# Kernel optimization log

Hardware: AMD Instinct MI355X
Metric: run time of the kernel (lower is better)

Reference implementation:

```python
import jax, jax.numpy as jnp
import numpy as np

DIM = 2048
N_HEADS = 32
N_KV_HEADS = 8
HEAD_DIM = DIM // N_HEADS  # 64
MAX_SEQ_LEN = 2048
ROPE_THETA = 10000.0
ROPE_SCALE = 1.0  # ("linear", 1.0)


def build_rope_cache(seq_len):
    # standard half-rotation RoPE cache with linear position scaling
    inv_freq = 1.0 / (ROPE_THETA ** (jnp.arange(0, HEAD_DIM, 2, dtype=jnp.float32) / HEAD_DIM))
    t = jnp.arange(seq_len, dtype=jnp.float32) / ROPE_SCALE
    freqs = jnp.outer(t, inv_freq)                      # [S, HD/2]
    emb = jnp.concatenate([freqs, freqs], axis=-1)      # [S, HD]
    return jnp.cos(emb), jnp.sin(emb)


def apply_rope(x, cos, sin):
    # x: [B, S, H, D]; cos/sin: [S, D]
    c = cos[None, :, None, :]
    s = sin[None, :, None, :]
    x1, x2 = jnp.split(x, 2, axis=-1)
    rot = jnp.concatenate([-x2, x1], axis=-1)           # rotate_half
    return x * c + rot * s


def setup_inputs() -> dict:
    key = jax.random.key(0)
    kx, kq, kk, kv, ko = jax.random.split(key, 5)
    B, S = 1, 2048
    x = jax.random.normal(kx, (B, S, DIM), dtype=jnp.float32)
    # nn.Linear weights stored [out_features, in_features]
    wq = jax.random.normal(kq, (DIM, DIM), dtype=jnp.float32) * 0.02
    wk = jax.random.normal(kk, (HEAD_DIM * N_KV_HEADS, DIM), dtype=jnp.float32) * 0.02
    wv = jax.random.normal(kv, (HEAD_DIM * N_KV_HEADS, DIM), dtype=jnp.float32) * 0.02
    wo = jax.random.normal(ko, (DIM, DIM), dtype=jnp.float32) * 0.02
    return {"x": x, "wq": wq, "wk": wk, "wv": wv, "wo": wo}


def reference(x, wq, wk, wv, wo):
    B, S, _ = x.shape
    g = N_HEADS // N_KV_HEADS  # GQA expand factor
    q = (x @ wq.T).reshape(B, S, N_HEADS, HEAD_DIM)
    k = (x @ wk.T).reshape(B, S, N_KV_HEADS, HEAD_DIM)
    v = (x @ wv.T).reshape(B, S, N_KV_HEADS, HEAD_DIM)
    cos, sin = build_rope_cache(S)
    q = apply_rope(q, cos, sin)
    k = apply_rope(k, cos, sin)
    # group q heads with their kv head instead of repeat_interleave on k/v
    q = q.transpose(0, 2, 1, 3).reshape(B, N_KV_HEADS, g, S, HEAD_DIM)
    k = k.transpose(0, 2, 1, 3)   # [B, Hkv, S, D]
    v = v.transpose(0, 2, 1, 3)
    scale = 1.0 / jnp.sqrt(jnp.asarray(HEAD_DIM, dtype=x.dtype))
    scores = jnp.einsum('bhgqd,bhkd->bhgqk', q, k) * scale  # [B,Hkv,g,S,S]
    causal = jnp.tril(jnp.ones((S, S), dtype=bool))
    scores = jnp.where(causal[None, None, None, :, :], scores, -jnp.inf)
    p = jax.nn.softmax(scores, axis=-1)
    out = jnp.einsum('bhgqk,bhkd->bhgqd', p, v)             # [B,Hkv,g,S,D]
    out = out.reshape(B, N_HEADS, S, HEAD_DIM).transpose(0, 2, 1, 3).reshape(B, S, DIM)
    return out @ wo.T
```

## Files before the change

### kernel.cpp

```cpp
#include <hip/hip_runtime.h>
#include <hip/hip_bf16.h>
#include <cstdint>
#include <cstddef>

#define DIM_ 2048
#define SLEN 2048
#define NQH 32
#define NKVH 8
#define HDIM 64
#define KVDIM 512

typedef __attribute__((ext_vector_type(8))) short short8;
typedef __attribute__((ext_vector_type(4))) float f32x4;
typedef __attribute__((ext_vector_type(16))) float f32x16;
typedef __attribute__((ext_vector_type(4))) unsigned int u32x4;

#define QSCALE 0.1803368801111243f

__device__ __forceinline__ unsigned short f2bf(float f) {
  unsigned u = __builtin_bit_cast(unsigned, f);
  u += 0x7FFFu + ((u >> 16) & 1u);
  return (unsigned short)(u >> 16);
}

__device__ __forceinline__ unsigned cvt_pk_bf16(float lo, float hi) {
  unsigned r;
  asm("v_cvt_pk_bf16_f32 %0, %1, %2" : "=v"(r) : "v"(lo), "v"(hi));
  return r;
}

__device__ __forceinline__ void gload_lds16(const void* g, void* l) {
  __builtin_amdgcn_global_load_lds(
      (const __attribute__((address_space(1))) void*)g,
      (__attribute__((address_space(3))) void*)l, 16, 0, 0);
}

__global__ void cvt_bf16_kernel(const float* __restrict__ in,
                                unsigned short* __restrict__ out, int n) {
  int i = (blockIdx.x * blockDim.x + threadIdx.x) * 8;
  if (i >= n) return;
  float4 a = *(const float4*)(in + i);
  float4 b = *(const float4*)(in + i + 4);
  ushort4 o0, o1;
  o0.x = f2bf(a.x); o0.y = f2bf(a.y); o0.z = f2bf(a.z); o0.w = f2bf(a.w);
  o1.x = f2bf(b.x); o1.y = f2bf(b.y); o1.z = f2bf(b.z); o1.w = f2bf(b.w);
  *(ushort4*)(out + i) = o0;
  *(ushort4*)(out + i + 4) = o1;
}

__global__ void rope_table_kernel(float* __restrict__ cosT, float* __restrict__ sinT) {
  int idx = blockIdx.x * blockDim.x + threadIdx.x;
  int s = idx >> 5, i = idx & 31;
  float inv = expf(-(float)i * (9.210340371976184f / 32.0f));
  float fr = (float)s * inv;
  cosT[idx] = cosf(fr);
  sinT[idx] = sinf(fr);
}

__global__ __launch_bounds__(512, 2)
void gemm_qkv(const unsigned short* __restrict__ A,
              const unsigned short* __restrict__ B,
              unsigned short* __restrict__ Qr,
              unsigned short* __restrict__ Kr,
              unsigned short* __restrict__ Vtp,
              const float* __restrict__ cosT,
              const float* __restrict__ sinT) {
  constexpr int K = DIM_;
  __shared__ unsigned short sA[128 * 32];
  __shared__ unsigned short sB[128 * 32];
  const int tid = threadIdx.x;
  const int wv = tid >> 6, ln = tid & 63;
  const int row0 = blockIdx.x * 128;
  const int col0 = blockIdx.y * 128;
  const int wr = (wv >> 1) * 32, wc = (wv & 1) * 64;
  const int lrow = ln & 15, lk = (ln >> 4) * 8;
  const int rr = tid >> 2, cc = (tid & 3) * 8;
  f32x4 acc[2][4] = {};

  for (int kt = 0; kt < K; kt += 32) {
    gload_lds16(A + (size_t)(row0 + rr) * K + kt + cc, sA + wv * 512);
    gload_lds16(B + (size_t)(col0 + rr) * K + kt + cc, sB + wv * 512);
    __syncthreads();
    short8 af[2], bfr[4];
#pragma unroll
    for (int m = 0; m < 2; ++m)
      af[m] = *(const short8*)(sA + (wr + m * 16 + lrow) * 32 + lk);
#pragma unroll
    for (int n = 0; n < 4; ++n)
      bfr[n] = *(const short8*)(sB + (wc + n * 16 + lrow) * 32 + lk);
#pragma unroll
    for (int m = 0; m < 2; ++m)
#pragma unroll
      for (int n = 0; n < 4; ++n)
        acc[m][n] = __builtin_amdgcn_mfma_f32_16x16x32_bf16(af[m], bfr[n],
                                                            acc[m][n], 0, 0, 0);
    __syncthreads();
  }
  const int orow = (ln >> 4) * 4;
  const int by = blockIdx.y;
  if (by < 16) {
#pragma unroll
    for (int m = 0; m < 2; ++m)
#pragma unroll
      for (int j = 0; j < 4; ++j) {
        const int s = row0 + wr + m * 16 + orow + j;
#pragma unroll
        for (int n = 0; n < 2; ++n) {
          const int d1 = n * 16 + lrow;
          const float cv = cosT[s * 32 + d1], sv = sinT[s * 32 + d1];
          const float x1 = acc[m][n][j], x2 = acc[m][n + 2][j];
          const size_t base = (size_t)s * DIM_ + col0 + wc + d1;
          Qr[base] = f2bf((x1 * cv - x2 * sv) * QSCALE);
          Qr[base + 32] = f2bf((x2 * cv + x1 * sv) * QSCALE);
        }
      }
  } else if (by < 20) {
    const int cb = col0 - 2048;
#pragma unroll
    for (int m = 0; m < 2; ++m)
#pragma unroll
      for (int j = 0; j < 4; ++j) {
        const int s = row0 + wr + m * 16 + orow + j;
#pragma unroll
        for (int n = 0; n < 2; ++n) {
          const int d1 = n * 16 + lrow;
          const float cv = cosT[s * 32 + d1], sv = sinT[s * 32 + d1];
          const float x1 = acc[m][n][j], x2 = acc[m][n + 2][j];
          const size_t base = (size_t)s * KVDIM + cb + wc + d1;
          Kr[base] = f2bf(x1 * cv - x2 * sv);
          Kr[base + 32] = f2bf(x2 * cv + x1 * sv);
        }
      }
  } else {
    const int cb = col0 - 2560;
#pragma unroll
    for (int m = 0; m < 2; ++m)
#pragma unroll
      for (int n = 0; n < 4; ++n)
#pragma unroll
        for (int j = 0; j < 4; ++j) {
          const int s = row0 + wr + m * 16 + orow + j;
          const int vc = cb + wc + n * 16 + lrow;
          Vtp[(size_t)vc * SLEN + s] = f2bf(acc[m][n][j]);
        }
  }
}

__global__ __launch_bounds__(512, 2)
void gemm_bt_f32(const unsigned short* __restrict__ A,
                 const unsigned short* __restrict__ B, float* __restrict__ C) {
  constexpr int K = DIM_;
  __shared__ unsigned short sA[128 * 32];
  __shared__ unsigned short sB[128 * 32];
  const int tid = threadIdx.x;
  const int wv = tid >> 6, ln = tid & 63;
  const int row0 = blockIdx.x * 128;
  const int col0 = blockIdx.y * 128;
  const int wr = (wv >> 1) * 32, wc = (wv & 1) * 64;
  const int lrow = ln & 15, lk = (ln >> 4) * 8;
  const int rr = tid >> 2, cc = (tid & 3) * 8;
  f32x4 acc[2][4] = {};
  for (int kt = 0; kt < K; kt += 32) {
    gload_lds16(A + (size_t)(row0 + rr) * K + kt + cc, sA + wv * 512);
    gload_lds16(B + (size_t)(col0 + rr) * K + kt + cc, sB + wv * 512);
    __syncthreads();
    short8 af[2], bfr[4];
#pragma unroll
    for (int m = 0; m < 2; ++m)
      af[m] = *(const short8*)(sA + (wr + m * 16 + lrow) * 32 + lk);
#pragma unroll
    for (int n = 0; n < 4; ++n)
      bfr[n] = *(const short8*)(sB + (wc + n * 16 + lrow) * 32 + lk);
#pragma unroll
    for (int m = 0; m < 2; ++m)
#pragma unroll
      for (int n = 0; n < 4; ++n)
        acc[m][n] = __builtin_amdgcn_mfma_f32_16x16x32_bf16(af[m], bfr[n],
                                                            acc[m][n], 0, 0, 0);
    __syncthreads();
  }
  const int orow = (ln >> 4) * 4;
#pragma unroll
  for (int m = 0; m < 2; ++m)
#pragma unroll
    for (int n = 0; n < 4; ++n)
#pragma unroll
      for (int j = 0; j < 4; ++j)
        C[(size_t)(row0 + wr + m * 16 + orow + j) * DIM_ + col0 + wc + n * 16 + lrow] =
            acc[m][n][j];
}

__global__ __launch_bounds__(256, 3)
void attn3_kernel(const unsigned short* __restrict__ Q,
                  const unsigned short* __restrict__ Kc,
                  const unsigned short* __restrict__ Vt,
                  unsigned short* __restrict__ AO) {
  __shared__ __align__(16) char smem[32768];
  const int c = 15 - blockIdx.x, h = blockIdx.y;
  const int kvh = h >> 2;
  const int tid = threadIdx.x;
  const int w = tid >> 6, l = tid & 63;
  const int l31 = l & 31, hi = l >> 5;
  const int kvcol = kvh * HDIM;
  const int nt = (c + 1) * 2;
  const int wq0 = c * 128 + w * 32;
  const int qrow = wq0 + l31;

  int srow[2], scolb[2];
#pragma unroll
  for (int r = 0; r < 2; ++r) {
    int L = (r * 256 + tid) * 16;
    int row = L >> 7;
    srow[r] = row;
    scolb[r] = (L & 127) ^ ((row & 7) << 4);
  }

  short8 qf[4];
  {
    const unsigned short* qp = Q + (size_t)qrow * DIM_ + h * HDIM + hi * 8;
#pragma unroll
    for (int dblk = 0; dblk < 4; ++dblk) qf[dblk] = *(const short8*)(qp + dblk * 16);
  }
  f32x16 o[2] = {};
  float mrun = -1e30f, lrun = 0.f;

#pragma unroll
  for (int r = 0; r < 2; ++r) {
    gload_lds16((const char*)Kc + (((size_t)srow[r] * KVDIM + kvcol) << 1) + scolb[r],
                smem + r * 4096 + w * 1024);
    gload_lds16((const char*)Vt + (((size_t)(kvcol + srow[r]) * SLEN) << 1) + scolb[r],
                smem + 16384 + r * 4096 + w * 1024);
  }
  __syncthreads();

  for (int t = 0; t < nt; ++t) {
    const int cur = t & 1;
    const int k0 = t * 64;
    if (t + 1 < nt) {
      const int nb = cur ^ 1;
      const int k0n = k0 + 64;
#pragma unroll
      for (int r = 0; r < 2; ++r) {
        gload_lds16((const char*)Kc + (((size_t)(k0n + srow[r]) * KVDIM + kvcol) << 1) + scolb[r],
                    smem + nb * 8192 + r * 4096 + w * 1024);
        gload_lds16((const char*)Vt + (((size_t)(kvcol + srow[r]) * SLEN + k0n) << 1) + scolb[r],
                    smem + 16384 + nb * 8192 + r * 4096 + w * 1024);
      }
    }
    if (k0 <= wq0 + 31) {
      const char* sK = smem + cur * 8192;
      const char* sV = smem + 16384 + cur * 8192;
      f32x16 s0 = {}, s1 = {};
      __builtin_amdgcn_s_setprio(1);
#pragma unroll
      for (int dblk = 0; dblk < 4; ++dblk) {
        const int colb = (dblk * 32 + hi * 16) ^ ((l31 & 7) << 4);
        short8 kf0 = *(const short8*)(sK + l31 * 128 + colb);
        short8 kf1 = *(const short8*)(sK + (32 + l31) * 128 + colb);
        s0 = __builtin_amdgcn_mfma_f32_32x32x16_bf16(kf0, qf[dblk], s0, 0, 0, 0);
        s1 = __builtin_amdgcn_mfma_f32_32x32x16_bf16(kf1, qf[dblk], s1, 0, 0, 0);
      }
      __builtin_amdgcn_s_setprio(0);

      float p[32];
#pragma unroll
      for (int r = 0; r < 16; ++r) { p[r] = s0[r]; p[16 + r] = s1[r]; }
      if (k0 + 63 > wq0) {
#pragma unroll
        for (int r = 0; r < 16; ++r) {
          const int ka = k0 + (r & 3) + 8 * (r >> 2) + 4 * hi;
          if (ka > qrow) p[r] = -1e30f;
          if (ka + 32 > qrow) p[16 + r] = -1e30f;
        }
      }
      float t16[16];
#pragma unroll
      for (int i = 0; i < 16; ++i) t16[i] = fmaxf(p[i], p[i + 16]);
#pragma unroll
      for (int i = 0; i < 8; ++i) t16[i] = fmaxf(t16[i], t16[i + 8]);
#pragma unroll
      for (int i = 0; i < 4; ++i) t16[i] = fmaxf(t16[i], t16[i + 4]);
      float pmax = fmaxf(fmaxf(t16[0], t16[1]), fmaxf(t16[2], t16[3]));
      pmax = fmaxf(pmax, __shfl_xor(pmax, 32));
      if (!__all(pmax - mrun <= 8.0f)) {
        const float mnew = fmaxf(mrun, pmax);
        const float alpha = exp2f(mrun - mnew);
        mrun = mnew;
        lrun *= alpha;
#pragma unroll
        for (int r = 0; r < 16; ++r) { o[0][r] *= alpha; o[1][r] *= alpha; }
      }
#pragma unroll
      for (int i = 0; i < 32; ++i) p[i] = exp2f(p[i] - mrun);
      float u16[16];
#pragma unroll
      for (int i = 0; i < 16; ++i) u16[i] = p[i] + p[i + 16];
#pragma unroll
      for (int i = 0; i < 8; ++i) u16[i] += u16[i + 8];
#pragma unroll
      for (int i = 0; i < 4; ++i) u16[i] += u16[i + 4];
      float rs = (u16[0] + u16[1]) + (u16[2] + u16[3]);
      rs += __shfl_xor(rs, 32);
      lrun += rs;

      unsigned pa[8], pb[8];
#pragma unroll
      for (int i = 0; i < 8; ++i) {
        pa[i] = cvt_pk_bf16(p[i * 4 + 0], p[i * 4 + 1]);
        pb[i] = cvt_pk_bf16(p[i * 4 + 2], p[i * 4 + 3]);
      }
      __builtin_amdgcn_s_setprio(1);
#pragma unroll
      for (int kb = 0; kb < 4; ++kb) {
        const int i0 = (kb >> 1) * 4 + (kb & 1) * 2;
        const int i1 = i0 + 1;
        unsigned w0 = pa[i0], w2 = pa[i1];
        asm("v_permlane32_swap_b32 %0, %1" : "+v"(w0), "+v"(w2));
        unsigned w1 = pb[i0], w3 = pb[i1];
        asm("v_permlane32_swap_b32 %0, %1" : "+v"(w1), "+v"(w3));
        u32x4 uu = {w0, w1, w2, w3};
        short8 pf = __builtin_bit_cast(short8, uu);
        const int colb = (kb * 32 + hi * 16) ^ ((l31 & 7) << 4);
        short8 vf0 = *(const short8*)(sV + l31 * 128 + colb);
        short8 vf1 = *(const short8*)(sV + (32 + l31) * 128 + colb);
        o[0] = __builtin_amdgcn_mfma_f32_32x32x16_bf16(vf0, pf, o[0], 0, 0, 0);
        o[1] = __builtin_amdgcn_mfma_f32_32x32x16_bf16(vf1, pf, o[1], 0, 0, 0);
      }
      __builtin_amdgcn_s_setprio(0);
    }
    __syncthreads();
  }

  const float inv = 1.0f / lrun;
  char* tw = smem + w * 4096;
#pragma unroll
  for (int db = 0; db < 2; ++db)
#pragma unroll
    for (int g = 0; g < 4; ++g) {
      ushort4 v;
      v.x = f2bf(o[db][g * 4 + 0] * inv);
      v.y = f2bf(o[db][g * 4 + 1] * inv);
      v.z = f2bf(o[db][g * 4 + 2] * inv);
      v.w = f2bf(o[db][g * 4 + 3] * inv);
      const int d0 = db * 32 + g * 8 + hi * 4;
      *(ushort4*)(tw + l31 * 128 + ((d0 * 2) ^ ((l31 & 7) << 4))) = v;
    }
  {
    const int rr = l >> 1, cc = (l & 1) * 32;
    unsigned short* ap = AO + (size_t)(c * 128 + w * 32 + rr) * DIM_ + h * HDIM + cc;
#pragma unroll
    for (int pq = 0; pq < 4; ++pq) {
      const int colb = ((cc + pq * 8) * 2) ^ ((rr & 7) << 4);
      short8 v = *(const short8*)(tw + rr * 128 + colb);
      *(short8*)(ap + pq * 8) = v;
    }
  }
}

extern "C" void kernel_launch(void* const* d_in, const int* in_sizes, int n_in,
                              void* d_out, int out_size, void* d_ws, size_t ws_size,
                              hipStream_t stream) {
  const float* x  = (const float*)d_in[0];
  const float* wq = (const float*)d_in[1];
  const float* wk = (const float*)d_in[2];
  const float* wv = (const float*)d_in[3];
  const float* wo = (const float*)d_in[4];
  float* out = (float*)d_out;
  char* ws = (char*)d_ws;
  const size_t MB = 1u << 20;
  unsigned short* bx   = (unsigned short*)(ws + 0 * MB);
  unsigned short* bqkv = (unsigned short*)(ws + 8 * MB);
  unsigned short* bwo  = (unsigned short*)(ws + 20 * MB);
  unsigned short* Qr   = (unsigned short*)(ws + 28 * MB);
  unsigned short* Kr   = (unsigned short*)(ws + 36 * MB);
  unsigned short* Vt   = (unsigned short*)(ws + 38 * MB);
  unsigned short* AO   = (unsigned short*)(ws + 40 * MB);
  float* cosT = (float*)(ws + 48 * MB);
  float* sinT = (float*)(ws + 48 * MB + 256 * 1024);

  rope_table_kernel<<<SLEN * 32 / 256, 256, 0, stream>>>(cosT, sinT);
  cvt_bf16_kernel<<<(2048 * 2048 / 8) / 256, 256, 0, stream>>>(x, bx, 2048 * 2048);
  cvt_bf16_kernel<<<(2048 * 2048 / 8) / 256, 256, 0, stream>>>(wq, bqkv, 2048 * 2048);
  cvt_bf16_kernel<<<(512 * 2048 / 8) / 256, 256, 0, stream>>>(wk, bqkv + 2048 * 2048, 512 * 2048);
  cvt_bf16_kernel<<<(512 * 2048 / 8) / 256, 256, 0, stream>>>(wv, bqkv + 2560 * 2048, 512 * 2048);
  cvt_bf16_kernel<<<(2048 * 2048 / 8) / 256, 256, 0, stream>>>(wo, bwo, 2048 * 2048);

  gemm_qkv<<<dim3(16, 24), 512, 0, stream>>>(bx, bqkv, Qr, Kr, Vt, cosT, sinT);

  attn3_kernel<<<dim3(16, 32), 256, 0, stream>>>(Qr, Kr, Vt, AO);

  gemm_bt_f32<<<dim3(16, 16), 512, 0, stream>>>(AO, bwo, out);
}
```

Measured before the change: 257.5 us.

## Double-buffer GEMM K tiles and load attention K/V directly into registers

Both bf16 GEMMs now use K-tiles of 64 with a double-buffered, XOR-swizzled LDS stage, so the next tile's global load overlaps the current tile's MFMAs and one barrier per iteration is removed. The attention kernel drops LDS staging entirely: each wave loads K fragments straight from global memory into registers, prefetching the next tile, and loads V fragments per tile. Each wave now runs only as many tiles as its own causal extent needs. Blocks are remapped onto a 1D grid so the four query heads sharing a KV head are adjacent, for L2 reuse. The costs are more register pressure (launch bounds drop to 2 blocks), redundant global K/V reads across waves, and larger LDS use in the GEMMs.

```diff
diff --git a/kernel.cpp b/kernel.cpp
--- a/kernel.cpp
+++ b/kernel.cpp
@@ -57,6 +57,40 @@
   sinT[idx] = sinf(fr);
 }
 
+#define GSTAGE(buf, kt)                                                        \
+  do {                                                                         \
+    _Pragma("unroll") for (int r = 0; r < 2; ++r) {                            \
+      const int L = r * 512 + tid;                                             \
+      const int row = L >> 3;                                                  \
+      const int scb = ((L & 7) * 16) ^ ((row & 7) << 4);                       \
+      gload_lds16((const char*)A + ((size_t)(row0 + row) * DIM_ + kt) * 2 + scb, \
+                  sA[buf] + (size_t)(r * 512 + wv * 64) * 8);                  \
+      gload_lds16((const char*)B + ((size_t)(col0 + row) * DIM_ + kt) * 2 + scb, \
+                  sB[buf] + (size_t)(r * 512 + wv * 64) * 8);                  \
+    }                                                                          \
+  } while (0)
+
+#define GCOMPUTE(cur)                                                          \
+  do {                                                                         \
+    _Pragma("unroll") for (int ks = 0; ks < 2; ++ks) {                         \
+      short8 af[2], bfr[4];                                                    \
+      _Pragma("unroll") for (int m = 0; m < 2; ++m) {                          \
+        const int row = wr + m * 16 + lrow;                                    \
+        const int cB = (ks * 64 + lkb) ^ ((row & 7) << 4);                     \
+        af[m] = *(const short8*)(sA[cur] + row * 64 + (cB >> 1));              \
+      }                                                                        \
+      _Pragma("unroll") for (int n = 0; n < 4; ++n) {                          \
+        const int row = wc + n * 16 + lrow;                                    \
+        const int cB = (ks * 64 + lkb) ^ ((row & 7) << 4);                     \
+        bfr[n] = *(const short8*)(sB[cur] + row * 64 + (cB >> 1));             \
+      }                                                                        \
+      _Pragma("unroll") for (int m = 0; m < 2; ++m)                            \
+          _Pragma("unroll") for (int n = 0; n < 4; ++n) acc[m][n] =            \
+              __builtin_amdgcn_mfma_f32_16x16x32_bf16(af[m], bfr[n],           \
+                                                      acc[m][n], 0, 0, 0);     \
+    }                                                                          \
+  } while (0)
+
 __global__ __launch_bounds__(512, 2)
 void gemm_qkv(const unsigned short* __restrict__ A,
               const unsigned short* __restrict__ B,
@@ -65,36 +99,21 @@
               unsigned short* __restrict__ Vtp,
               const float* __restrict__ cosT,
               const float* __restrict__ sinT) {
-  constexpr int K = DIM_;
-  __shared__ unsigned short sA[128 * 32];
-  __shared__ unsigned short sB[128 * 32];
+  __shared__ unsigned short sA[2][128 * 64];
+  __shared__ unsigned short sB[2][128 * 64];
   const int tid = threadIdx.x;
   const int wv = tid >> 6, ln = tid & 63;
   const int row0 = blockIdx.x * 128;
   const int col0 = blockIdx.y * 128;
   const int wr = (wv >> 1) * 32, wc = (wv & 1) * 64;
-  const int lrow = ln & 15, lk = (ln >> 4) * 8;
-  const int rr = tid >> 2, cc = (tid & 3) * 8;
+  const int lrow = ln & 15, lkb = (ln >> 4) * 16;
   f32x4 acc[2][4] = {};
 
-  for (int kt = 0; kt < K; kt += 32) {
-    gload_lds16(A + (size_t)(row0 + rr) * K + kt + cc, sA + wv * 512);
-    gload_lds16(B + (size_t)(col0 + rr) * K + kt + cc, sB + wv * 512);
+  GSTAGE(0, 0);
+  for (int t = 0; t < 32; ++t) {
     __syncthreads();
-    short8 af[2], bfr[4];
-#pragma unroll
-    for (int m = 0; m < 2; ++m)
-      af[m] = *(const short8*)(sA + (wr + m * 16 + lrow) * 32 + lk);
-#pragma unroll
-    for (int n = 0; n < 4; ++n)
-      bfr[n] = *(const short8*)(sB + (wc + n * 16 + lrow) * 32 + lk);
-#pragma unroll
-    for (int m = 0; m < 2; ++m)
-#pragma unroll
-      for (int n = 0; n < 4; ++n)
-        acc[m][n] = __builtin_amdgcn_mfma_f32_16x16x32_bf16(af[m], bfr[n],
-                                                            acc[m][n], 0, 0, 0);
-    __syncthreads();
+    if (t + 1 < 32) GSTAGE((t + 1) & 1, (t + 1) * 64);
+    GCOMPUTE(t & 1);
   }
   const int orow = (ln >> 4) * 4;
   const int by = blockIdx.y;
@@ -149,35 +168,21 @@
 __global__ __launch_bounds__(512, 2)
 void gemm_bt_f32(const unsigned short* __restrict__ A,
                  const unsigned short* __restrict__ B, float* __restrict__ C) {
-  constexpr int K = DIM_;
-  __shared__ unsigned short sA[128 * 32];
-  __shared__ unsigned short sB[128 * 32];
+  __shared__ unsigned short sA[2][128 * 64];
+  __shared__ unsigned short sB[2][128 * 64];
   const int tid = threadIdx.x;
   const int wv = tid >> 6, ln = tid & 63;
   const int row0 = blockIdx.x * 128;
   const int col0 = blockIdx.y * 128;
   const int wr = (wv >> 1) * 32, wc = (wv & 1) * 64;
-  const int lrow = ln & 15, lk = (ln >> 4) * 8;
-  const int rr = tid >> 2, cc = (tid & 3) * 8;
+  const int lrow = ln & 15, lkb = (ln >> 4) * 16;
   f32x4 acc[2][4] = {};
-  for (int kt = 0; kt < K; kt += 32) {
-    gload_lds16(A + (size_t)(row0 + rr) * K + kt + cc, sA + wv * 512);
-    gload_lds16(B + (size_t)(col0 + rr) * K + kt + cc, sB + wv * 512);
+
+  GSTAGE(0, 0);
+  for (int t = 0; t < 32; ++t) {
     __syncthreads();
-    short8 af[2], bfr[4];
-#pragma unroll
-    for (int m = 0; m < 2; ++m)
-      af[m] = *(const short8*)(sA + (wr + m * 16 + lrow) * 32 + lk);
-#pragma unroll
-    for (int n = 0; n < 4; ++n)
-      bfr[n] = *(const short8*)(sB + (wc + n * 16 + lrow) * 32 + lk);
-#pragma unroll
-    for (int m = 0; m < 2; ++m)
-#pragma unroll
-      for (int n = 0; n < 4; ++n)
-        acc[m][n] = __builtin_amdgcn_mfma_f32_16x16x32_bf16(af[m], bfr[n],
-                                                            acc[m][n], 0, 0, 0);
-    __syncthreads();
+    if (t + 1 < 32) GSTAGE((t + 1) & 1, (t + 1) * 64);
+    GCOMPUTE(t & 1);
   }
   const int orow = (ln >> 4) * 4;
 #pragma unroll
@@ -190,145 +195,138 @@
             acc[m][n][j];
 }
 
-__global__ __launch_bounds__(256, 3)
-void attn3_kernel(const unsigned short* __restrict__ Q,
+__global__ __launch_bounds__(256, 2)
+void attn4_kernel(const unsigned short* __restrict__ Q,
                   const unsigned short* __restrict__ Kc,
                   const unsigned short* __restrict__ Vt,
                   unsigned short* __restrict__ AO) {
-  __shared__ __align__(16) char smem[32768];
-  const int c = 15 - blockIdx.x, h = blockIdx.y;
-  const int kvh = h >> 2;
+  __shared__ __align__(16) char smem[16384];
+  const int id = blockIdx.x;
+  const int kvh = id & 7, hg = (id >> 3) & 3;
+  const int c = 15 - (id >> 5);
+  const int h = kvh * 4 + hg;
   const int tid = threadIdx.x;
   const int w = tid >> 6, l = tid & 63;
   const int l31 = l & 31, hi = l >> 5;
-  const int kvcol = kvh * HDIM;
-  const int nt = (c + 1) * 2;
   const int wq0 = c * 128 + w * 32;
   const int qrow = wq0 + l31;
-
-  int srow[2], scolb[2];
-#pragma unroll
-  for (int r = 0; r < 2; ++r) {
-    int L = (r * 256 + tid) * 16;
-    int row = L >> 7;
-    srow[r] = row;
-    scolb[r] = (L & 127) ^ ((row & 7) << 4);
-  }
+  const int ntw = (wq0 + 95) >> 6;
+
+  const unsigned short* Kb = Kc + kvh * HDIM;
+  const unsigned short* Vb = Vt + (size_t)kvh * HDIM * SLEN;
 
   short8 qf[4];
   {
     const unsigned short* qp = Q + (size_t)qrow * DIM_ + h * HDIM + hi * 8;
 #pragma unroll
-    for (int dblk = 0; dblk < 4; ++dblk) qf[dblk] = *(const short8*)(qp + dblk * 16);
+    for (int d = 0; d < 4; ++d) qf[d] = *(const short8*)(qp + d * 16);
   }
   f32x16 o[2] = {};
   float mrun = -1e30f, lrun = 0.f;
 
-#pragma unroll
-  for (int r = 0; r < 2; ++r) {
-    gload_lds16((const char*)Kc + (((size_t)srow[r] * KVDIM + kvcol) << 1) + scolb[r],
-                smem + r * 4096 + w * 1024);
-    gload_lds16((const char*)Vt + (((size_t)(kvcol + srow[r]) * SLEN) << 1) + scolb[r],
-                smem + 16384 + r * 4096 + w * 1024);
-  }
-  __syncthreads();
-
-  for (int t = 0; t < nt; ++t) {
-    const int cur = t & 1;
+  auto loadK = [&](short8* kf, int t) {
+    const unsigned short* kp = Kb + (size_t)(t * 64 + l31) * KVDIM + hi * 8;
+#pragma unroll
+    for (int d = 0; d < 4; ++d) {
+      kf[d] = *(const short8*)(kp + d * 16);
+      kf[4 + d] = *(const short8*)(kp + 32 * KVDIM + d * 16);
+    }
+  };
+
+  auto body = [&](int t, const short8* kf) {
     const int k0 = t * 64;
-    if (t + 1 < nt) {
-      const int nb = cur ^ 1;
-      const int k0n = k0 + 64;
-#pragma unroll
-      for (int r = 0; r < 2; ++r) {
-        gload_lds16((const char*)Kc + (((size_t)(k0n + srow[r]) * KVDIM + kvcol) << 1) + scolb[r],
-                    smem + nb * 8192 + r * 4096 + w * 1024);
-        gload_lds16((const char*)Vt + (((size_t)(kvcol + srow[r]) * SLEN + k0n) << 1) + scolb[r],
-                    smem + 16384 + nb * 8192 + r * 4096 + w * 1024);
+    short8 vf0[4], vf1[4];
+    {
+      const unsigned short* vp = Vb + (size_t)l31 * SLEN + k0 + hi * 8;
+#pragma unroll
+      for (int d = 0; d < 4; ++d) {
+        vf0[d] = *(const short8*)(vp + d * 16);
+        vf1[d] = *(const short8*)(vp + (size_t)32 * SLEN + d * 16);
       }
     }
-    if (k0 <= wq0 + 31) {
-      const char* sK = smem + cur * 8192;
-      const char* sV = smem + 16384 + cur * 8192;
-      f32x16 s0 = {}, s1 = {};
-      __builtin_amdgcn_s_setprio(1);
-#pragma unroll
-      for (int dblk = 0; dblk < 4; ++dblk) {
-        const int colb = (dblk * 32 + hi * 16) ^ ((l31 & 7) << 4);
-        short8 kf0 = *(const short8*)(sK + l31 * 128 + colb);
-        short8 kf1 = *(const short8*)(sK + (32 + l31) * 128 + colb);
-        s0 = __builtin_amdgcn_mfma_f32_32x32x16_bf16(kf0, qf[dblk], s0, 0, 0, 0);
-        s1 = __builtin_amdgcn_mfma_f32_32x32x16_bf16(kf1, qf[dblk], s1, 0, 0, 0);
+    f32x16 s0 = {}, s1 = {};
+    __builtin_amdgcn_s_setprio(1);
+#pragma unroll
+    for (int d = 0; d < 4; ++d) {
+      s0 = __builtin_amdgcn_mfma_f32_32x32x16_bf16(kf[d], qf[d], s0, 0, 0, 0);
+      s1 = __builtin_amdgcn_mfma_f32_32x32x16_bf16(kf[4 + d], qf[d], s1, 0, 0, 0);
+    }
+    __builtin_amdgcn_s_setprio(0);
+
+    float p[32];
+#pragma unroll
+    for (int r = 0; r < 16; ++r) { p[r] = s0[r]; p[16 + r] = s1[r]; }
+    if (k0 + 63 > wq0) {
+#pragma unroll
+      for (int r = 0; r < 16; ++r) {
+        const int ka = k0 + (r & 3) + 8 * (r >> 2) + 4 * hi;
+        if (ka > qrow) p[r] = -1e30f;
+        if (ka + 32 > qrow) p[16 + r] = -1e30f;
       }
-      __builtin_amdgcn_s_setprio(0);
-
-      float p[32];
-#pragma unroll
-      for (int r = 0; r < 16; ++r) { p[r] = s0[r]; p[16 + r] = s1[r]; }
-      if (k0 + 63 > wq0) {
-#pragma unroll
-        for (int r = 0; r < 16; ++r) {
-          const int ka = k0 + (r & 3) + 8 * (r >> 2) + 4 * hi;
-          if (ka > qrow) p[r] = -1e30f;
-          if (ka + 32 > qrow) p[16 + r] = -1e30f;
-        }
-      }
-      float t16[16];
-#pragma unroll
-      for (int i = 0; i < 16; ++i) t16[i] = fmaxf(p[i], p[i + 16]);
-#pragma unroll
-      for (int i = 0; i < 8; ++i) t16[i] = fmaxf(t16[i], t16[i + 8]);
-#pragma unroll
-      for (int i = 0; i < 4; ++i) t16[i] = fmaxf(t16[i], t16[i + 4]);
-      float pmax = fmaxf(fmaxf(t16[0], t16[1]), fmaxf(t16[2], t16[3]));
-      pmax = fmaxf(pmax, __shfl_xor(pmax, 32));
-      if (!__all(pmax - mrun <= 8.0f)) {
-        const float mnew = fmaxf(mrun, pmax);
-        const float alpha = exp2f(mrun - mnew);
-        mrun = mnew;
-        lrun *= alpha;
-#pragma unroll
-        for (int r = 0; r < 16; ++r) { o[0][r] *= alpha; o[1][r] *= alpha; }
-      }
-#pragma unroll
-      for (int i = 0; i < 32; ++i) p[i] = exp2f(p[i] - mrun);
-      float u16[16];
-#pragma unroll
-      for (int i = 0; i < 16; ++i) u16[i] = p[i] + p[i + 16];
-#pragma unroll
-      for (int i = 0; i < 8; ++i) u16[i] += u16[i + 8];
-#pragma unroll
-      for (int i = 0; i < 4; ++i) u16[i] += u16[i + 4];
-      float rs = (u16[0] + u16[1]) + (u16[2] + u16[3]);
-      rs += __shfl_xor(rs, 32);
-      lrun += rs;
-
-      unsigned pa[8], pb[8];
-#pragma unroll
-      for (int i = 0; i < 8; ++i) {
-        pa[i] = cvt_pk_bf16(p[i * 4 + 0], p[i * 4 + 1]);
-        pb[i] = cvt_pk_bf16(p[i * 4 + 2], p[i * 4 + 3]);
-      }
-      __builtin_amdgcn_s_setprio(1);
-#pragma unroll
-      for (int kb = 0; kb < 4; ++kb) {
-        const int i0 = (kb >> 1) * 4 + (kb & 1) * 2;
-        const int i1 = i0 + 1;
-        unsigned w0 = pa[i0], w2 = pa[i1];
-        asm("v_permlane32_swap_b32 %0, %1" : "+v"(w0), "+v"(w2));
-        unsigned w1 = pb[i0], w3 = pb[i1];
-        asm("v_permlane32_swap_b32 %0, %1" : "+v"(w1), "+v"(w3));
-        u32x4 uu = {w0, w1, w2, w3};
-        short8 pf = __builtin_bit_cast(short8, uu);
-        const int colb = (kb * 32 + hi * 16) ^ ((l31 & 7) << 4);
-        short8 vf0 = *(const short8*)(sV + l31 * 128 + colb);
-        short8 vf1 = *(const short8*)(sV + (32 + l31) * 128 + colb);
-        o[0] = __builtin_amdgcn_mfma_f32_32x32x16_bf16(vf0, pf, o[0], 0, 0, 0);
-        o[1] = __builtin_amdgcn_mfma_f32_32x32x16_bf16(vf1, pf, o[1], 0, 0, 0);
-      }
-      __builtin_amdgcn_s_setprio(0);
-    }
-    __syncthreads();
+    }
+    float t16[16];
+#pragma unroll
+    for (int i = 0; i < 16; ++i) t16[i] = fmaxf(p[i], p[i + 16]);
+#pragma unroll
+    for (int i = 0; i < 8; ++i) t16[i] = fmaxf(t16[i], t16[i + 8]);
+#pragma unroll
+    for (int i = 0; i < 4; ++i) t16[i] = fmaxf(t16[i], t16[i + 4]);
+    float pmax = fmaxf(fmaxf(t16[0], t16[1]), fmaxf(t16[2], t16[3]));
+    pmax = fmaxf(pmax, __shfl_xor(pmax, 32));
+    if (!__all(pmax - mrun <= 8.0f)) {
+      const float mnew = fmaxf(mrun, pmax);
+      const float alpha = exp2f(mrun - mnew);
+      mrun = mnew;
+      lrun *= alpha;
+#pragma unroll
+      for (int r = 0; r < 16; ++r) { o[0][r] *= alpha; o[1][r] *= alpha; }
+    }
+#pragma unroll
+    for (int i = 0; i < 32; ++i) p[i] = exp2f(p[i] - mrun);
+    float u16[16];
+#pragma unroll
+    for (int i = 0; i < 16; ++i) u16[i] = p[i] + p[i + 16];
+#pragma unroll
+    for (int i = 0; i < 8; ++i) u16[i] += u16[i + 8];
+#pragma unroll
+    for (int i = 0; i < 4; ++i) u16[i] += u16[i + 4];
+    float rs = (u16[0] + u16[1]) + (u16[2] + u16[3]);
+    rs += __shfl_xor(rs, 32);
+    lrun += rs;
+
+    unsigned pa[8], pb[8];
+#pragma unroll
+    for (int i = 0; i < 8; ++i) {
+      pa[i] = cvt_pk_bf16(p[i * 4 + 0], p[i * 4 + 1]);
+      pb[i] = cvt_pk_bf16(p[i * 4 + 2], p[i * 4 + 3]);
+    }
+    __builtin_amdgcn_s_setprio(1);
+#pragma unroll
+    for (int kb = 0; kb < 4; ++kb) {
+      const int i0 = (kb >> 1) * 4 + (kb & 1) * 2;
+      const int i1 = i0 + 1;
+      unsigned w0 = pa[i0], w2 = pa[i1];
+      asm("v_permlane32_swap_b32 %0, %1" : "+v"(w0), "+v"(w2));
+      unsigned w1 = pb[i0], w3 = pb[i1];
+      asm("v_permlane32_swap_b32 %0, %1" : "+v"(w1), "+v"(w3));
+      u32x4 uu = {w0, w1, w2, w3};
+      short8 pf = __builtin_bit_cast(short8, uu);
+      o[0] = __builtin_amdgcn_mfma_f32_32x32x16_bf16(vf0[kb], pf, o[0], 0, 0, 0);
+      o[1] = __builtin_amdgcn_mfma_f32_32x32x16_bf16(vf1[kb], pf, o[1], 0, 0, 0);
+    }
+    __builtin_amdgcn_s_setprio(0);
+  };
+
+  short8 ka[8], kb_[8];
+  loadK(ka, 0);
+  int t = 0;
+  for (;;) {
+    if (t + 1 < ntw) loadK(kb_, t + 1);
+    body(t, ka);
+    if (++t >= ntw) break;
+    if (t + 1 < ntw) loadK(ka, t + 1);
+    body(t, kb_);
+    if (++t >= ntw) break;
   }
 
   const float inv = 1.0f / lrun;
@@ -387,7 +385,7 @@
 
   gemm_qkv<<<dim3(16, 24), 512, 0, stream>>>(bx, bqkv, Qr, Kr, Vt, cosT, sinT);
 
-  attn3_kernel<<<dim3(16, 32), 256, 0, stream>>>(Qr, Kr, Vt, AO);
+  attn4_kernel<<<512, 256, 0, stream>>>(Qr, Kr, Vt, AO);
 
   gemm_bt_f32<<<dim3(16, 16), 512, 0, stream>>>(AO, bwo, out);
 }
```

After: 262.1 us. No clear change (+1.8%).
